# Optimization experiments

Hardware: AMD Instinct MI355X
Metric: run time of the kernel (lower is better)

## Reference

```python
import jax, jax.numpy as jnp
import numpy as np

N_NODES = 50000
N_EDGES = 800000
NFEAT, NHID, NCLASS = 256, 64, 2


def _deg_norm(idx, n_nodes, dtype):
    deg = jax.ops.segment_sum(jnp.ones(idx.shape[0], dtype=dtype), idx, num_segments=n_nodes)
    return jax.lax.rsqrt(jnp.maximum(deg, 1.0))


def gcn_layer(x, W, b, src, dst, n_nodes):
    # DGL GraphConv, norm='both': h = D_in^{-1/2} * Agg( D_out^{-1/2} * x ) W + b
    # weight applied before aggregation (in_feats >= out_feats path); math-equivalent.
    norm_src = _deg_norm(src, n_nodes, x.dtype)  # out-degree norm of source nodes
    norm_dst = _deg_norm(dst, n_nodes, x.dtype)  # in-degree norm of dest nodes
    h = (x * norm_src[:, None]) @ W              # [N, out]
    agg = jax.ops.segment_sum(h[src], dst, num_segments=n_nodes)  # gather + scatter-add
    return agg * norm_dst[:, None] + b


def setup_inputs() -> dict:
    key = jax.random.key(0)
    k1, k2, k3, k4, k5, k6, k7 = jax.random.split(key, 7)
    x = jax.random.normal(k1, (N_NODES, NFEAT), dtype=jnp.float32)
    src = jax.random.randint(k2, (N_EDGES,), 0, N_NODES, dtype=jnp.int64)
    dst = jax.random.randint(k3, (N_EDGES,), 0, N_NODES, dtype=jnp.int64)
    # Glorot-style init like DGL GraphConv
    W1 = jax.random.normal(k4, (NFEAT, NHID), dtype=jnp.float32) * (2.0 / (NFEAT + NHID)) ** 0.5
    b1 = jnp.zeros((NHID,), dtype=jnp.float32)
    W2 = jax.random.normal(k5, (NHID, NCLASS), dtype=jnp.float32) * (2.0 / (NHID + NCLASS)) ** 0.5
    b2 = jnp.zeros((NCLASS,), dtype=jnp.float32)
    return {"x": x, "src": src, "dst": dst, "W1": W1, "b1": b1, "W2": W2, "b2": b2}


def reference(x, src, dst, W1, b1, W2, b2):
    h = jax.nn.relu(gcn_layer(x, W1, b1, src, dst, N_NODES))
    # dropout=False -> p=0, no-op
    logits = gcn_layer(h, W2, b2, src, dst, N_NODES)
    return jax.nn.log_softmax(logits, axis=1)
```

## Files before the change

### kernel.cpp

```cpp
#include <hip/hip_runtime.h>
#include <math.h>

#define N_NODES 50000
#define N_EDGES 800000
#define NFEAT 256
#define NHID 64
#define NCLASS 2

#define DB 64
#define NDB 782
#define BCAP 1536
#define EPB 4096
#define NB_EDGE ((N_EDGES + EPB - 1) / EPB)
#define NSUB 16
#define SUBCAP 160
#define CSTR 8

#define OFF_CURD 0
#define OFF_CURS 100096
#define OFF_RBD  200192
#define OFF_NDST 300192
#define OFF_NSRC 350192
#define OFF_W1T  400192
#define OFF_DPK  408384
#define OFF_SV6  2410304
#define OFF_CSR  2910784
#define OFF_HF32 4111936
#define OFF_HB   7311936
#define OFF_H2   8911936

typedef __attribute__((ext_vector_type(8))) short bf16x8;
typedef __attribute__((ext_vector_type(4))) float f32x4;

static __device__ __forceinline__ unsigned short f2bf(float f) {
    union { float f; unsigned int u; } v; v.f = f;
    return (unsigned short)((v.u + 0x8000u) >> 16);
}
static __device__ __forceinline__ unsigned int pk2bf(float f0, float f1) {
    union { float f; unsigned int u; } a, b; a.f = f0; b.f = f1;
    return __builtin_amdgcn_perm(b.u + 0x8000u, a.u + 0x8000u, 0x07060302u);
}
static __device__ __forceinline__ float bflo(unsigned int u) {
    union { unsigned int x; float f; } v; v.x = u << 16; return v.f;
}
static __device__ __forceinline__ float bfhi(unsigned int u) {
    union { unsigned int x; float f; } v; v.x = u & 0xffff0000u; return v.f;
}

#define INIT_CUR (2 * NDB * NSUB * CSTR)
#define INIT_N (INIT_CUR + NFEAT * NHID)
__global__ __launch_bounds__(256) void init_kernel(const float* __restrict__ W1,
                                                   int* __restrict__ cursors,
                                                   unsigned short* __restrict__ w1t) {
    int g = blockIdx.x * 256 + threadIdx.x;
    if (g < INIT_CUR) {
        cursors[g] = 0;
    } else if (g < INIT_N) {
        int idx = g - INIT_CUR;
        int k = idx >> 6, n = idx & 63;
        w1t[n * NFEAT + k] = f2bf(W1[idx]);
    }
}

struct SgShared { int hd[NDB], bd[NDB], cd[NDB], hs[NDB], bs[NDB], cs[NDB]; };
__global__ __launch_bounds__(256) void sg_kernel(const int* __restrict__ src,
                                                 const int* __restrict__ dst,
                                                 const float* __restrict__ x,
                                                 const unsigned short* __restrict__ w1t,
                                                 int* __restrict__ cur_d,
                                                 int* __restrict__ cur_s,
                                                 int* __restrict__ dpk,
                                                 unsigned char* __restrict__ sv6,
                                                 float* __restrict__ hf32) {
    __shared__ SgShared su;
    int t = threadIdx.x;
    int bid = blockIdx.x;
    if (bid % 5 == 0) {
        int chunk = bid / 5;
        int sub = chunk & (NSUB - 1);
        for (int i = t; i < NDB; i += 256) { su.hd[i] = 0; su.cd[i] = 0; su.hs[i] = 0; su.cs[i] = 0; }
        __syncthreads();
        int base = chunk * EPB;
        int ls[16], ld[16];
#pragma unroll
        for (int i = 0; i < 16; ++i) {
            int e = base + t + i * 256;
            ls[i] = (e < N_EDGES) ? src[e] : -1;
            ld[i] = (e < N_EDGES) ? dst[e] : -1;
            if (ld[i] >= 0) {
                atomicAdd(&su.hd[ld[i] >> 6], 1);
                atomicAdd(&su.hs[ls[i] >> 6], 1);
            }
        }
        __syncthreads();
        for (int i = t; i < NDB; i += 256) {
            if (su.hd[i]) su.bd[i] = atomicAdd(&cur_d[(sub * NDB + i) * CSTR], su.hd[i]);
            if (su.hs[i]) su.bs[i] = atomicAdd(&cur_s[(sub * NDB + i) * CSTR], su.hs[i]);
        }
        __syncthreads();
#pragma unroll
        for (int i = 0; i < 16; ++i) {
            if (ld[i] >= 0) {
                int bin = ld[i] >> 6;
                int pos = su.bd[bin] + atomicAdd(&su.cd[bin], 1);
                dpk[(bin * NSUB + sub) * SUBCAP + pos] = (ls[i] << 6) | (ld[i] & 63);
                int sbin = ls[i] >> 6;
                int spos = su.bs[sbin] + atomicAdd(&su.cs[sbin], 1);
                sv6[(sbin * NSUB + sub) * SUBCAP + spos] = (unsigned char)(ls[i] & 63);
            }
        }
    } else {
        const int g = bid - 1 - bid / 5;
        if (g >= NDB) return;
        const int row0 = g * 64;
        const int w = t >> 6;
        const int l = t & 63;
        const int m = l & 15;
        const int q = l >> 4;
        int grow = row0 + w * 16 + m;
        const float* xr = &x[(size_t)((grow < N_NODES) ? grow : 0) * NFEAT];
        float4 av[16];
#pragma unroll
        for (int i = 0; i < 8; ++i) {
            av[2 * i]     = *(const float4*)(xr + i * 32 + q * 8);
            av[2 * i + 1] = *(const float4*)(xr + i * 32 + q * 8 + 4);
        }
        f32x4 acc[4] = {{0.f, 0.f, 0.f, 0.f}, {0.f, 0.f, 0.f, 0.f},
                        {0.f, 0.f, 0.f, 0.f}, {0.f, 0.f, 0.f, 0.f}};
#pragma unroll
        for (int c8 = 0; c8 < 8; ++c8) {
            int k0 = c8 * 32 + q * 8;
            union { bf16x8 v; unsigned int u[4]; } a;
            a.u[0] = pk2bf(av[2 * c8].x, av[2 * c8].y);
            a.u[1] = pk2bf(av[2 * c8].z, av[2 * c8].w);
            a.u[2] = pk2bf(av[2 * c8 + 1].x, av[2 * c8 + 1].y);
            a.u[3] = pk2bf(av[2 * c8 + 1].z, av[2 * c8 + 1].w);
#pragma unroll
            for (int ct = 0; ct < 4; ++ct) {
                bf16x8 bb = *(const bf16x8*)(&w1t[(ct * 16 + m) * NFEAT + k0]);
                acc[ct] = __builtin_amdgcn_mfma_f32_16x16x32_bf16(a.v, bb, acc[ct], 0, 0, 0);
            }
        }
#pragma unroll
        for (int reg = 0; reg < 4; ++reg) {
            int r = row0 + w * 16 + q * 4 + reg;
            if (r < N_NODES) {
#pragma unroll
                for (int ct = 0; ct < 4; ++ct)
                    hf32[(size_t)r * NHID + ct * 16 + m] = acc[ct][reg];
            }
        }
    }
}

union FinShared {
    struct { int ebuf[BCAP]; int hist4[256]; int hist[64]; int seg[64]; int cur[64]; } d;
    struct { int hist4[256]; float nss[64]; } s;
};
__global__ __launch_bounds__(256) void fin_kernel(const int* __restrict__ cur_d,
                                                  const int* __restrict__ cur_s,
                                                  const int* __restrict__ dpk,
                                                  const unsigned char* __restrict__ sv6,
                                                  const float* __restrict__ hf32,
                                                  int2* __restrict__ rbdeg,
                                                  float* __restrict__ norm_dst,
                                                  float* __restrict__ norm_src,
                                                  int* __restrict__ csr,
                                                  unsigned short* __restrict__ hb) {
    __shared__ FinShared su;
    int t = threadIdx.x;
    int role = blockIdx.x & 1;
    int b = blockIdx.x >> 1;

    if (role == 0) {
        su.s.hist4[t] = 0;
        __syncthreads();
        int sub4 = (t & 3) * 64;
        for (int sub = 0; sub < NSUB; ++sub) {
            int c = cur_s[(sub * NDB + b) * CSTR];
            c = (c < SUBCAP) ? c : SUBCAP;
            int gb = (b * NSUB + sub) * SUBCAP;
            for (int j = t; j < c; j += 256) atomicAdd(&su.s.hist4[sub4 + sv6[gb + j]], 1);
        }
        __syncthreads();
        if (t < 64) {
            int gid = b * 64 + t;
            int v = su.s.hist4[t] + su.s.hist4[64 + t] + su.s.hist4[128 + t] + su.s.hist4[192 + t];
            float ns = rsqrtf(fmaxf((float)v, 1.0f));
            su.s.nss[t] = ns;
            if (gid < N_NODES) norm_src[gid] = ns;
        }
        __syncthreads();
        for (int i = t; i < 1024; i += 256) {
            int n8 = i >> 4;
            int q = i & 15;
            int gid = b * 64 + n8;
            if (gid < N_NODES) {
                float s = su.s.nss[n8];
                float4 v = *(const float4*)(&hf32[(size_t)gid * NHID + q * 4]);
                uint2 o;
                o.x = pk2bf(v.x * s, v.y * s);
                o.y = pk2bf(v.z * s, v.w * s);
                *(uint2*)(&hb[(size_t)gid * NHID + q * 4]) = o;
            }
        }
    } else {
        int base = b * BCAP;
        if (t < 64) { su.d.hist[t] = 0; su.d.cur[t] = 0; }
        su.d.hist4[t] = 0;
        int off = 0;
        for (int sub = 0; sub < NSUB; ++sub) {
            int c = cur_d[(sub * NDB + b) * CSTR];
            c = (c < SUBCAP) ? c : SUBCAP;
            int gb = (b * NSUB + sub) * SUBCAP;
            for (int j = t; j < c; j += 256) su.d.ebuf[off + j] = dpk[gb + j];
            off += c;
        }
        int cnt = off;
        __syncthreads();
        int sub4 = (t & 3) * 64;
        for (int j = t; j < cnt; j += 256) atomicAdd(&su.d.hist4[sub4 + (su.d.ebuf[j] & 63)], 1);
        __syncthreads();
        if (t < 64) {
            int v = su.d.hist4[t] + su.d.hist4[64 + t] + su.d.hist4[128 + t] + su.d.hist4[192 + t];
            su.d.hist[t] = v;
            su.d.seg[t] = v;
        }
        __syncthreads();
#pragma unroll
        for (int offp = 1; offp < 64; offp <<= 1) {
            int xv = 0;
            if (t < 64 && t >= offp) xv = su.d.seg[t - offp];
            __syncthreads();
            if (t < 64) su.d.seg[t] += xv;
            __syncthreads();
        }
        if (t < 64) {
            int v = su.d.hist[t];
            int excl = su.d.seg[t] - v;
            int gid = b * 64 + t;
            if (gid < N_NODES) {
                rbdeg[gid] = make_int2(base + excl, v);
                norm_dst[gid] = rsqrtf(fmaxf((float)v, 1.0f));
            }
            su.d.seg[t] = excl;
        }
        __syncthreads();
        for (int j = t; j < cnt; j += 256) {
            int p = su.d.ebuf[j];
            int dlow = p & 63;
            int pos = base + su.d.seg[dlow] + atomicAdd(&su.d.cur[dlow], 1);
            csr[pos] = ((unsigned)p) >> 6;
        }
    }
}

__global__ __launch_bounds__(256) void fused1_kernel(const int2* __restrict__ rbdeg,
                                                     const int* __restrict__ csr,
                                                     const unsigned short* __restrict__ hb,
                                                     const float* __restrict__ norm_dst,
                                                     const float* __restrict__ norm_src,
                                                     const float* __restrict__ b1,
                                                     const float* __restrict__ W2,
                                                     float* __restrict__ h2) {
    int gtid = blockIdx.x * blockDim.x + threadIdx.x;
    int node = gtid >> 6;
    int lane = gtid & 63;
    if (node >= N_NODES) return;
    int e8 = lane >> 3, fg = lane & 7;
    int2 rd = rbdeg[node];
    int beg = rd.x;
    int end = beg + rd.y;
    float a0 = 0.f, a1 = 0.f, a2 = 0.f, a3 = 0.f, a4 = 0.f, a5 = 0.f, a6 = 0.f, a7 = 0.f;
    for (int j = beg; j < end; j += 32) {
        int j0 = j + e8, j1 = j0 + 8, j2 = j0 + 16, j3 = j0 + 24;
        uint4 u0 = make_uint4(0u, 0u, 0u, 0u), u1 = make_uint4(0u, 0u, 0u, 0u);
        uint4 u2 = make_uint4(0u, 0u, 0u, 0u), u3 = make_uint4(0u, 0u, 0u, 0u);
        if (j0 < end) u0 = *(const uint4*)(&hb[(size_t)csr[j0] * NHID + fg * 8]);
        if (j1 < end) u1 = *(const uint4*)(&hb[(size_t)csr[j1] * NHID + fg * 8]);
        if (j2 < end) u2 = *(const uint4*)(&hb[(size_t)csr[j2] * NHID + fg * 8]);
        if (j3 < end) u3 = *(const uint4*)(&hb[(size_t)csr[j3] * NHID + fg * 8]);
        a0 += bflo(u0.x) + bflo(u1.x) + bflo(u2.x) + bflo(u3.x);
        a1 += bfhi(u0.x) + bfhi(u1.x) + bfhi(u2.x) + bfhi(u3.x);
        a2 += bflo(u0.y) + bflo(u1.y) + bflo(u2.y) + bflo(u3.y);
        a3 += bfhi(u0.y) + bfhi(u1.y) + bfhi(u2.y) + bfhi(u3.y);
        a4 += bflo(u0.z) + bflo(u1.z) + bflo(u2.z) + bflo(u3.z);
        a5 += bfhi(u0.z) + bfhi(u1.z) + bfhi(u2.z) + bfhi(u3.z);
        a6 += bflo(u0.w) + bflo(u1.w) + bflo(u2.w) + bflo(u3.w);
        a7 += bfhi(u0.w) + bfhi(u1.w) + bfhi(u2.w) + bfhi(u3.w);
    }
#pragma unroll
    for (int off = 8; off <= 32; off <<= 1) {
        a0 += __shfl_xor(a0, off, 64);
        a1 += __shfl_xor(a1, off, 64);
        a2 += __shfl_xor(a2, off, 64);
        a3 += __shfl_xor(a3, off, 64);
        a4 += __shfl_xor(a4, off, 64);
        a5 += __shfl_xor(a5, off, 64);
        a6 += __shfl_xor(a6, off, 64);
        a7 += __shfl_xor(a7, off, 64);
    }
    float nd = norm_dst[node], ns = norm_src[node];
    float4 bv0 = *(const float4*)(&b1[fg * 8]);
    float4 bv1 = *(const float4*)(&b1[fg * 8 + 4]);
    float4 w0 = *(const float4*)(&W2[fg * 16 + 0]);
    float4 w1 = *(const float4*)(&W2[fg * 16 + 4]);
    float4 w2v = *(const float4*)(&W2[fg * 16 + 8]);
    float4 w3 = *(const float4*)(&W2[fg * 16 + 12]);
    float h0 = fmaxf(fmaf(a0, nd, bv0.x), 0.f) * ns;
    float h1 = fmaxf(fmaf(a1, nd, bv0.y), 0.f) * ns;
    float h2f = fmaxf(fmaf(a2, nd, bv0.z), 0.f) * ns;
    float h3 = fmaxf(fmaf(a3, nd, bv0.w), 0.f) * ns;
    float h4 = fmaxf(fmaf(a4, nd, bv1.x), 0.f) * ns;
    float h5 = fmaxf(fmaf(a5, nd, bv1.y), 0.f) * ns;
    float h6 = fmaxf(fmaf(a6, nd, bv1.z), 0.f) * ns;
    float h7 = fmaxf(fmaf(a7, nd, bv1.w), 0.f) * ns;
    float p0 = h0 * w0.x + h1 * w0.z + h2f * w1.x + h3 * w1.z +
               h4 * w2v.x + h5 * w2v.z + h6 * w3.x + h7 * w3.z;
    float p1 = h0 * w0.y + h1 * w0.w + h2f * w1.y + h3 * w1.w +
               h4 * w2v.y + h5 * w2v.w + h6 * w3.y + h7 * w3.w;
#pragma unroll
    for (int off = 1; off <= 4; off <<= 1) {
        p0 += __shfl_xor(p0, off, 64);
        p1 += __shfl_xor(p1, off, 64);
    }
    if (lane == 0) *(float2*)(&h2[node * 2]) = make_float2(p0, p1);
}

__global__ __launch_bounds__(256) void fused2_kernel(const int2* __restrict__ rbdeg,
                                                     const int* __restrict__ csr,
                                                     const float* __restrict__ h2,
                                                     const float* __restrict__ norm_dst,
                                                     const float* __restrict__ b2,
                                                     float* __restrict__ out) {
    int gtid = blockIdx.x * blockDim.x + threadIdx.x;
    int n = gtid >> 4;
    int l16 = gtid & 15;
    if (n >= N_NODES) return;
    int2 rd = rbdeg[n];
    int beg = rd.x, end = rd.x + rd.y;
    float s0 = 0.f, s1 = 0.f;
    for (int j = beg + l16; j < end; j += 16) {
        float2 v = *(const float2*)(&h2[csr[j] * 2]);
        s0 += v.x;
        s1 += v.y;
    }
#pragma unroll
    for (int off = 1; off <= 8; off <<= 1) {
        s0 += __shfl_xor(s0, off, 16);
        s1 += __shfl_xor(s1, off, 16);
    }
    if (l16 == 0) {
        float nd = norm_dst[n];
        float l0 = fmaf(s0, nd, b2[0]);
        float l1 = fmaf(s1, nd, b2[1]);
        float m = fmaxf(l0, l1);
        float lse = m + logf(expf(l0 - m) + expf(l1 - m));
        *(float2*)(&out[n * 2]) = make_float2(l0 - lse, l1 - lse);
    }
}

extern "C" void kernel_launch(void* const* d_in, const int* in_sizes, int n_in,
                              void* d_out, int out_size, void* d_ws, size_t ws_size,
                              hipStream_t stream) {
    const float* x  = (const float*)d_in[0];
    const int* src  = (const int*)d_in[1];
    const int* dst  = (const int*)d_in[2];
    const float* W1 = (const float*)d_in[3];
    const float* b1 = (const float*)d_in[4];
    const float* W2 = (const float*)d_in[5];
    const float* b2 = (const float*)d_in[6];
    float* out = (float*)d_out;
    float* ws  = (float*)d_ws;
    int*   wsi = (int*)d_ws;

    int*   cur_d    = wsi + OFF_CURD;
    int*   cur_s    = wsi + OFF_CURS;
    int2*  rbdeg    = (int2*)(wsi + OFF_RBD);
    float* norm_dst = ws + OFF_NDST;
    float* norm_src = ws + OFF_NSRC;
    unsigned short* w1t = (unsigned short*)(wsi + OFF_W1T);
    int*   dpk      = wsi + OFF_DPK;
    unsigned char* sv6 = (unsigned char*)(wsi + OFF_SV6);
    int*   csr      = wsi + OFF_CSR;
    float* hf32     = ws + OFF_HF32;
    unsigned short* hb = (unsigned short*)(wsi + OFF_HB);
    float* h2       = ws + OFF_H2;

    init_kernel<<<(INIT_N + 255) / 256, 256, 0, stream>>>(W1, cur_d, w1t);
    sg_kernel<<<NB_EDGE * 5, 256, 0, stream>>>(src, dst, x, w1t, cur_d, cur_s, dpk, sv6, hf32);
    fin_kernel<<<NDB * 2, 256, 0, stream>>>(cur_d, cur_s, dpk, sv6, hf32,
                                            rbdeg, norm_dst, norm_src, csr, hb);
    {
        long long threads = (long long)N_NODES * 64;
        fused1_kernel<<<(int)((threads + 255) / 256), 256, 0, stream>>>(
            rbdeg, csr, hb, norm_dst, norm_src, b1, W2, h2);
    }
    {
        long long threads = (long long)N_NODES * 16;
        fused2_kernel<<<(int)((threads + 255) / 256), 256, 0, stream>>>(
            rbdeg, csr, h2, norm_dst, b2, out);
    }
}
```

Before: 171.0 us.

## Halve edges per binning block, double sub-buckets, flatten fin gather loops

Edge-binning blocks now handle 2048 edges each instead of 4096, and the number of sub-buckets rises from 16 to 32 with a smaller per-sub capacity. The interleave ratio changes from 1-in-5 to 1-in-3 binning blocks so that more binning blocks run alongside the GEMM blocks. In fin_kernel the per-sub serial loops become one flat loop over all sub slots, using shared prefix offsets and lengths, which removes serialized global count reads. A sched_barrier is added after the x loads and an occupancy hint is set; the workspace grows, and each fin block now scans more mostly-empty slots.

```diff
diff --git a/kernel.cpp b/kernel.cpp
--- a/kernel.cpp
+++ b/kernel.cpp
@@ -10,24 +10,24 @@
 #define DB 64
 #define NDB 782
 #define BCAP 1536
-#define EPB 4096
+#define EPB 2048
 #define NB_EDGE ((N_EDGES + EPB - 1) / EPB)
-#define NSUB 16
-#define SUBCAP 160
+#define NSUB 32
+#define SUBCAP 128
 #define CSTR 8
 
 #define OFF_CURD 0
-#define OFF_CURS 100096
-#define OFF_RBD  200192
-#define OFF_NDST 300192
-#define OFF_NSRC 350192
-#define OFF_W1T  400192
-#define OFF_DPK  408384
-#define OFF_SV6  2410304
-#define OFF_CSR  2910784
-#define OFF_HF32 4111936
-#define OFF_HB   7311936
-#define OFF_H2   8911936
+#define OFF_CURS 200192
+#define OFF_RBD  400384
+#define OFF_NDST 500384
+#define OFF_NSRC 550384
+#define OFF_W1T  600384
+#define OFF_DPK  608576
+#define OFF_SV6  3811648
+#define OFF_CSR  4612416
+#define OFF_HF32 5813568
+#define OFF_HB   9013568
+#define OFF_H2   10613568
 
 typedef __attribute__((ext_vector_type(8))) short bf16x8;
 typedef __attribute__((ext_vector_type(4))) float f32x4;
@@ -63,27 +63,27 @@
 }
 
 struct SgShared { int hd[NDB], bd[NDB], cd[NDB], hs[NDB], bs[NDB], cs[NDB]; };
-__global__ __launch_bounds__(256) void sg_kernel(const int* __restrict__ src,
-                                                 const int* __restrict__ dst,
-                                                 const float* __restrict__ x,
-                                                 const unsigned short* __restrict__ w1t,
-                                                 int* __restrict__ cur_d,
-                                                 int* __restrict__ cur_s,
-                                                 int* __restrict__ dpk,
-                                                 unsigned char* __restrict__ sv6,
-                                                 float* __restrict__ hf32) {
+__global__ __launch_bounds__(256, 4) void sg_kernel(const int* __restrict__ src,
+                                                    const int* __restrict__ dst,
+                                                    const float* __restrict__ x,
+                                                    const unsigned short* __restrict__ w1t,
+                                                    int* __restrict__ cur_d,
+                                                    int* __restrict__ cur_s,
+                                                    int* __restrict__ dpk,
+                                                    unsigned char* __restrict__ sv6,
+                                                    float* __restrict__ hf32) {
     __shared__ SgShared su;
     int t = threadIdx.x;
     int bid = blockIdx.x;
-    if (bid % 5 == 0) {
-        int chunk = bid / 5;
+    if (bid % 3 == 0) {
+        int chunk = bid / 3;
         int sub = chunk & (NSUB - 1);
         for (int i = t; i < NDB; i += 256) { su.hd[i] = 0; su.cd[i] = 0; su.hs[i] = 0; su.cs[i] = 0; }
         __syncthreads();
         int base = chunk * EPB;
-        int ls[16], ld[16];
-#pragma unroll
-        for (int i = 0; i < 16; ++i) {
+        int ls[8], ld[8];
+#pragma unroll
+        for (int i = 0; i < 8; ++i) {
             int e = base + t + i * 256;
             ls[i] = (e < N_EDGES) ? src[e] : -1;
             ld[i] = (e < N_EDGES) ? dst[e] : -1;
@@ -99,7 +99,7 @@
         }
         __syncthreads();
 #pragma unroll
-        for (int i = 0; i < 16; ++i) {
+        for (int i = 0; i < 8; ++i) {
             if (ld[i] >= 0) {
                 int bin = ld[i] >> 6;
                 int pos = su.bd[bin] + atomicAdd(&su.cd[bin], 1);
@@ -110,7 +110,7 @@
             }
         }
     } else {
-        const int g = bid - 1 - bid / 5;
+        const int g = bid - 1 - bid / 3;
         if (g >= NDB) return;
         const int row0 = g * 64;
         const int w = t >> 6;
@@ -125,6 +125,7 @@
             av[2 * i]     = *(const float4*)(xr + i * 32 + q * 8);
             av[2 * i + 1] = *(const float4*)(xr + i * 32 + q * 8 + 4);
         }
+        __builtin_amdgcn_sched_barrier(0);
         f32x4 acc[4] = {{0.f, 0.f, 0.f, 0.f}, {0.f, 0.f, 0.f, 0.f},
                         {0.f, 0.f, 0.f, 0.f}, {0.f, 0.f, 0.f, 0.f}};
 #pragma unroll
@@ -154,8 +155,9 @@
 }
 
 union FinShared {
-    struct { int ebuf[BCAP]; int hist4[256]; int hist[64]; int seg[64]; int cur[64]; } d;
-    struct { int hist4[256]; float nss[64]; } s;
+    struct { int ebuf[BCAP]; int hist4[256]; int hist[64]; int seg[64]; int cur[64];
+             int slen[NSUB]; int spre[NSUB + 1]; } d;
+    struct { int hist4[256]; float nss[64]; int slen[NSUB]; } s;
 };
 __global__ __launch_bounds__(256) void fin_kernel(const int* __restrict__ cur_d,
                                                   const int* __restrict__ cur_s,
@@ -174,13 +176,17 @@
 
     if (role == 0) {
         su.s.hist4[t] = 0;
+        if (t < NSUB) {
+            int c = cur_s[(t * NDB + b) * CSTR];
+            su.s.slen[t] = (c < SUBCAP) ? c : SUBCAP;
+        }
         __syncthreads();
         int sub4 = (t & 3) * 64;
-        for (int sub = 0; sub < NSUB; ++sub) {
-            int c = cur_s[(sub * NDB + b) * CSTR];
-            c = (c < SUBCAP) ? c : SUBCAP;
-            int gb = (b * NSUB + sub) * SUBCAP;
-            for (int j = t; j < c; j += 256) atomicAdd(&su.s.hist4[sub4 + sv6[gb + j]], 1);
+        int gbase = b * NSUB * SUBCAP;
+        for (int idx = t; idx < NSUB * SUBCAP; idx += 256) {
+            int sub = idx >> 7;
+            int j = idx & (SUBCAP - 1);
+            if (j < su.s.slen[sub]) atomicAdd(&su.s.hist4[sub4 + sv6[gbase + idx]], 1);
         }
         __syncthreads();
         if (t < 64) {
@@ -208,15 +214,26 @@
         int base = b * BCAP;
         if (t < 64) { su.d.hist[t] = 0; su.d.cur[t] = 0; }
         su.d.hist4[t] = 0;
-        int off = 0;
-        for (int sub = 0; sub < NSUB; ++sub) {
-            int c = cur_d[(sub * NDB + b) * CSTR];
-            c = (c < SUBCAP) ? c : SUBCAP;
-            int gb = (b * NSUB + sub) * SUBCAP;
-            for (int j = t; j < c; j += 256) su.d.ebuf[off + j] = dpk[gb + j];
-            off += c;
-        }
-        int cnt = off;
+        if (t < NSUB) {
+            int c = cur_d[(t * NDB + b) * CSTR];
+            su.d.slen[t] = (c < SUBCAP) ? c : SUBCAP;
+        }
+        __syncthreads();
+        if (t == 0) {
+            int acc = 0;
+#pragma unroll
+            for (int s = 0; s < NSUB; ++s) { su.d.spre[s] = acc; acc += su.d.slen[s]; }
+            su.d.spre[NSUB] = (acc < BCAP) ? acc : BCAP;
+        }
+        __syncthreads();
+        int gbase = b * NSUB * SUBCAP;
+        for (int idx = t; idx < NSUB * SUBCAP; idx += 256) {
+            int sub = idx >> 7;
+            int j = idx & (SUBCAP - 1);
+            int dstp = su.d.spre[sub] + j;
+            if (j < su.d.slen[sub] && dstp < BCAP) su.d.ebuf[dstp] = dpk[gbase + idx];
+        }
+        int cnt = su.d.spre[NSUB];
         __syncthreads();
         int sub4 = (t & 3) * 64;
         for (int j = t; j < cnt; j += 256) atomicAdd(&su.d.hist4[sub4 + (su.d.ebuf[j] & 63)], 1);
@@ -388,7 +405,7 @@
     float* h2       = ws + OFF_H2;
 
     init_kernel<<<(INIT_N + 255) / 256, 256, 0, stream>>>(W1, cur_d, w1t);
-    sg_kernel<<<NB_EDGE * 5, 256, 0, stream>>>(src, dst, x, w1t, cur_d, cur_s, dpk, sv6, hf32);
+    sg_kernel<<<NB_EDGE * 3, 256, 0, stream>>>(src, dst, x, w1t, cur_d, cur_s, dpk, sv6, hf32);
     fin_kernel<<<NDB * 2, 256, 0, stream>>>(cur_d, cur_s, dpk, sv6, hf32,
                                             rbdeg, norm_dst, norm_src, csr, hb);
     {
```

Result: no change. 172.4 us (+0.8%).
